# Kernel tuning notes

Measured on AMD Instinct MI355X. Metric: run time of the kernel, lower is better.

## Reference

```python
import math
import jax, jax.numpy as jnp
import numpy as np

EMBED = 512
HEADS = 2
HEAD_DIM = EMBED // HEADS


def setup_inputs() -> dict:
    key = jax.random.key(0)
    ks = jax.random.split(key, 10)
    s = 1.0 / math.sqrt(EMBED)
    return {
        "text_embeds": jax.random.normal(ks[0], (64, 32, EMBED), jnp.float32),
        "video_embeds": jax.random.normal(ks[1], (128, 64, EMBED), jnp.float32),
        "Wq": jax.random.normal(ks[2], (EMBED, EMBED), jnp.float32) * s,
        "bq": jnp.zeros((EMBED,), jnp.float32),
        "Wk": jax.random.normal(ks[3], (EMBED, EMBED), jnp.float32) * s,
        "bk": jnp.zeros((EMBED,), jnp.float32),
        "Wv": jax.random.normal(ks[4], (EMBED, EMBED), jnp.float32) * s,
        "bv": jnp.zeros((EMBED,), jnp.float32),
        "Wo": jax.random.normal(ks[5], (EMBED, EMBED), jnp.float32) * s,
        "bo": jnp.zeros((EMBED,), jnp.float32),
    }


def reference(text_embeds, video_embeds, Wq, bq, Wk, bk, Wv, bv, Wo, bo):
    num_texts, num_words, _ = text_embeds.shape
    num_vids, num_frames, _ = video_embeds.shape
    # projections (torch Linear: x @ W.T + b)
    q = (text_embeds @ Wq.T + bq).reshape(num_texts, num_words, HEADS, HEAD_DIM)
    k = (video_embeds @ Wk.T + bk).reshape(num_vids, num_frames, HEADS, HEAD_DIM)
    v = (video_embeds @ Wv.T + bv).reshape(num_vids, num_frames, HEADS, HEAD_DIM)
    # 5D cross attention logits: [vids, texts, heads, frames, words]
    logits = jnp.einsum('avhd,bthd->abhvt', k, q) / math.sqrt(HEAD_DIM)
    weights = jax.nn.softmax(logits, axis=3)  # softmax over frames
    attn = jnp.einsum('avhd,abhvt->abhtd', v, weights)  # [a,b,h,t,d]
    # faithful to torch: reshape (a,b,h,t,d) -> (a,b,t,h*d) in row-major order
    attn = attn.reshape(num_vids, num_texts, num_words, EMBED)
    attn = attn.mean(axis=0)  # [texts, words, embed]
    return attn @ Wo.T + bo
```

## Files before the change

kernel.cpp:

```cpp
#include <hip/hip_runtime.h>
#include <hip/hip_bf16.h>
#include <math.h>

#define EMBED  512
#define HEADS  2
#define HDIM   256
#define NTEXT  64
#define NWORD  32
#define NVID   128
#define NFRM   64

typedef __attribute__((ext_vector_type(8))) short      short8;
typedef __attribute__((ext_vector_type(8))) unsigned short ushort8;
typedef __attribute__((ext_vector_type(4))) float      float4v;
typedef __attribute__((ext_vector_type(4))) unsigned short ushort4v;

__device__ __forceinline__ unsigned short f2bf(float x) {
    __hip_bfloat16 h = __float2bfloat16(x);
    return *(unsigned short*)&h;
}
__device__ __forceinline__ float bf2f(unsigned short u) {
    __hip_bfloat16 h = *(__hip_bfloat16*)&u;
    return __bfloat162float(h);
}

__device__ __forceinline__ void gload_lds16(unsigned short* dst, const unsigned short* src) {
#if __has_builtin(__builtin_amdgcn_global_load_lds)
    __builtin_amdgcn_global_load_lds((const __attribute__((address_space(1))) void*)src,
                                     (__attribute__((address_space(3))) void*)dst,
                                     16, 0, 0);
#else
    *(ushort8*)dst = *(const ushort8*)src;
#endif
}

__global__ __launch_bounds__(256)
void cvt5(const float* __restrict__ s0, const float* __restrict__ s1,
          const float* __restrict__ s2, const float* __restrict__ s3,
          const float* __restrict__ s4, unsigned short* __restrict__ dst) {
    const int y = blockIdx.y;
    const float* s; size_t off; int n4;
    if (y == 0)      { s = s0; off = 0;       n4 = 262144;  }
    else if (y == 1) { s = s1; off = 1048576; n4 = 1048576; }
    else if (y == 2) { s = s2; off = 5242880; n4 = 65536;   }
    else if (y == 3) { s = s3; off = 5505024; n4 = 65536;   }
    else             { s = s4; off = 5767168; n4 = 65536;   }
    unsigned short* d = dst + off;
    for (int i = blockIdx.x * 256 + threadIdx.x; i < n4; i += 512 * 256) {
        float4v f = ((const float4v*)s)[i];
        ((ushort4v*)d)[i] = (ushort4v){f2bf(f.x), f2bf(f.y), f2bf(f.z), f2bf(f.w)};
    }
}

__global__ __launch_bounds__(256)
void proj_qkv(const unsigned short* __restrict__ text, const unsigned short* __restrict__ video,
              const unsigned short* __restrict__ Wqb, const float* __restrict__ bq,
              const unsigned short* __restrict__ Wkb, const float* __restrict__ bk,
              const unsigned short* __restrict__ Wvb, const float* __restrict__ bv,
              unsigned short* __restrict__ qout,
              unsigned short* __restrict__ Kgf, unsigned short* __restrict__ Vgf) {
    const int mb = blockIdx.x, nb = blockIdx.y;
    const int bj = nb * 128;
    const unsigned short *A, *W;
    const float* bias;
    int op, arow0, abase = 0;
    if (mb < 16)      { op = 0; A = text;  W = Wqb; bias = bq; arow0 = mb * 128; }
    else if (mb < 80) { op = 1; A = video; W = Wkb; bias = bk; abase = (mb - 16) * 2; arow0 = abase * 64; }
    else              { op = 2; A = video; W = Wvb; bias = bv; abase = (mb - 80) * 2; arow0 = abase * 64; }

    __shared__ __align__(16) unsigned char smem[65536];

    const int tid = threadIdx.x;
    const int w = tid >> 6, lane = tid & 63;
    const int lm = lane & 15, qd = lane >> 4;
    const int wr = w >> 1, wc = w & 1;

    float4v acc[4][4];
    #pragma unroll
    for (int rt = 0; rt < 4; ++rt)
        #pragma unroll
        for (int ct = 0; ct < 4; ++ct) acc[rt][ct] = (float4v){0.f, 0.f, 0.f, 0.f};

    auto STAGE = [&](int buf, int k0) {
        unsigned short* AbL = (unsigned short*)(smem + buf * 32768);
        unsigned short* WbL = (unsigned short*)(smem + buf * 32768 + 16384);
        #pragma unroll
        for (int it = 0; it < 4; ++it) {
            const int s = tid + it * 256;
            const int r = s >> 3, c8 = s & 7;
            const int sc = (c8 ^ (r & 7)) * 8;
            gload_lds16(&AbL[(size_t)s * 8], &A[(size_t)(arow0 + r) * 512 + k0 + sc]);
            gload_lds16(&WbL[(size_t)s * 8], &W[(size_t)(bj    + r) * 512 + k0 + sc]);
        }
    };

    STAGE(0, 0);
    __syncthreads();
    int cur = 0;
    for (int ks = 0; ks < 8; ++ks) {
        if (ks < 7) STAGE(cur ^ 1, (ks + 1) * 64);
        const unsigned short* AbL = (const unsigned short*)(smem + cur * 32768);
        const unsigned short* WbL = (const unsigned short*)(smem + cur * 32768 + 16384);
        #pragma unroll
        for (int kq = 0; kq < 2; ++kq) {
            const int scol = (kq * 32 + qd * 8) ^ ((lm & 7) * 8);
            short8 af[4], bf[4];
            #pragma unroll
            for (int rt = 0; rt < 4; ++rt)
                af[rt] = *(const short8*)&AbL[(wr * 64 + rt * 16 + lm) * 64 + scol];
            #pragma unroll
            for (int ct = 0; ct < 4; ++ct)
                bf[ct] = *(const short8*)&WbL[(wc * 64 + ct * 16 + lm) * 64 + scol];
            #pragma unroll
            for (int rt = 0; rt < 4; ++rt)
                #pragma unroll
                for (int ct = 0; ct < 4; ++ct)
                    acc[rt][ct] = __builtin_amdgcn_mfma_f32_16x16x32_bf16(af[rt], bf[ct], acc[rt][ct], 0, 0, 0);
        }
        __syncthreads();
        cur ^= 1;
    }

    if (op == 0) {
        #pragma unroll
        for (int rt = 0; rt < 4; ++rt)
            #pragma unroll
            for (int ct = 0; ct < 4; ++ct) {
                const int c = bj + wc * 64 + ct * 16 + lm;
                const float bb = bias[c];
                #pragma unroll
                for (int reg = 0; reg < 4; ++reg) {
                    const int r = arow0 + wr * 64 + rt * 16 + qd * 4 + reg;
                    qout[(size_t)r * 512 + c] = f2bf((acc[rt][ct][reg] + bb) * 0.0625f);
                }
            }
        return;
    }

    const int a   = abase + wr;
    const int bjs = bj + wc * 64;
    const int h      = bjs >> 8;
    const int bj_rel = bjs & 255;
    unsigned short (*Eb)[72] = (unsigned short (*)[72])(smem + w * 9216);
    const size_t base = ((size_t)(h * 128 + a)) * 16384;

    if (op == 1) {
        #pragma unroll
        for (int ct = 0; ct < 4; ++ct) {
            const int dl = ct * 16 + lm;
            const float bb = bias[bjs + dl];
            #pragma unroll
            for (int rt = 0; rt < 4; ++rt)
                #pragma unroll
                for (int reg = 0; reg < 4; ++reg)
                    Eb[rt * 16 + qd * 4 + reg][dl] = f2bf(acc[rt][ct][reg] + bb);
        }
        __syncthreads();
        #pragma unroll
        for (int it = 0; it < 8; ++it) {
            const int s = lane + it * 64;
            const int ntf = s >> 7, kqr = (s >> 6) & 1, l = s & 63;
            const int v = ntf * 16 + (l & 15);
            const int dl = kqr * 32 + (l >> 4) * 8;
            ushort8 val = *(const ushort8*)&Eb[v][dl];
            *(ushort8*)&Kgf[base + ((size_t)(ntf * 8 + (bj_rel >> 5) + kqr) * 64 + l) * 8] = val;
        }
    } else {
        #pragma unroll
        for (int ct = 0; ct < 4; ++ct) {
            const int dl = ct * 16 + lm;
            const float bb = bias[bjs + dl];
            #pragma unroll
            for (int rt = 0; rt < 4; ++rt)
                #pragma unroll
                for (int reg = 0; reg < 4; ++reg)
                    Eb[dl][rt * 16 + qd * 4 + reg] = f2bf(acc[rt][ct][reg] + bb);
        }
        __syncthreads();
        #pragma unroll
        for (int it = 0; it < 8; ++it) {
            const int s = lane + it * 64;
            const int ntr = s >> 7, kqv = (s >> 6) & 1, l = s & 63;
            const int dl = ntr * 16 + (l & 15);
            const int v0 = kqv * 32 + (l >> 4) * 8;
            ushort8 val = *(const ushort8*)&Eb[dl][v0];
            *(ushort8*)&Vgf[base + ((size_t)(((bj_rel >> 4) + ntr) * 2 + kqv) * 64 + l) * 8] = val;
        }
    }
}

__global__ __launch_bounds__(512, 2)
void attn9(const unsigned short* __restrict__ Kgf,
           const unsigned short* __restrict__ Vgf,
           const unsigned short* __restrict__ q,
           unsigned short* __restrict__ partg) {
    const int c  = blockIdx.x;
    const int h  = blockIdx.y;
    const int tg = blockIdx.z;
    const int tid = threadIdx.x;
    const int w = tid >> 6, lane = tid & 63;
    const int lm = lane & 15, qd = lane >> 4;
    const int wt = w >> 1;
    const int fh = w & 1;
    const int b = tg * 4 + wt;

    __shared__ __align__(16) unsigned short Kb[2][16384];
    __shared__ __align__(16) unsigned short Vb[2][16384];
    __shared__ __align__(16) unsigned short Pf[4][2][2][512];
    __shared__ __align__(16) float Ex[4][2][2][16][2];

    short8 qf[2][8];
    #pragma unroll
    for (int mt = 0; mt < 2; ++mt)
        #pragma unroll
        for (int kq = 0; kq < 8; ++kq)
            qf[mt][kq] = *(const short8*)
                &q[((size_t)(b * 32 + mt * 16 + lm)) * 512 + h * 256 + kq * 32 + qd * 8];

    float4v pacc[2][8];
    #pragma unroll
    for (int mt = 0; mt < 2; ++mt)
        #pragma unroll
        for (int nd = 0; nd < 8; ++nd) pacc[mt][nd] = (float4v){0.f, 0.f, 0.f, 0.f};

    const size_t vb0 = (size_t)(h * 128 + c * 16) * 16384;

    #pragma unroll
    for (int i = 0; i < 4; ++i) {
        const int s = tid + i * 512;
        gload_lds16(&Kb[0][(size_t)s * 8], &Kgf[vb0 + (size_t)s * 8]);
        gload_lds16(&Vb[0][(size_t)s * 8], &Vgf[vb0 + (size_t)s * 8]);
    }
    #pragma unroll
    for (int i = 0; i < 4; ++i) {
        const int s = tid + i * 512;
        gload_lds16(&Kb[1][(size_t)s * 8], &Kgf[vb0 + 16384 + (size_t)s * 8]);
        gload_lds16(&Vb[1][(size_t)s * 8], &Vgf[vb0 + 16384 + (size_t)s * 8]);
    }
    __syncthreads();

    for (int ai = 0; ai < 16; ++ai) {
        const int cur = ai & 1;

        float4v lacc[2][2];
        #pragma unroll
        for (int nt = 0; nt < 2; ++nt)
            #pragma unroll
            for (int mt = 0; mt < 2; ++mt) lacc[nt][mt] = (float4v){0.f, 0.f, 0.f, 0.f};
        #pragma unroll
        for (int kq = 0; kq < 8; ++kq) {
            #pragma unroll
            for (int nt = 0; nt < 2; ++nt) {
                const short8 kf = *(const short8*)
                    &Kb[cur][(((fh * 2 + nt) * 8 + kq) * 64 + lane) * 8];
                lacc[nt][0] = __builtin_amdgcn_mfma_f32_16x16x32_bf16(kf, qf[0][kq], lacc[nt][0], 0, 0, 0);
                lacc[nt][1] = __builtin_amdgcn_mfma_f32_16x16x32_bf16(kf, qf[1][kq], lacc[nt][1], 0, 0, 0);
            }
        }

        float m2[2], sv[2], e[2][2][4];
        #pragma unroll
        for (int mt = 0; mt < 2; ++mt) {
            float mm = lacc[0][mt][0];
            #pragma unroll
            for (int nt = 0; nt < 2; ++nt)
                #pragma unroll
                for (int r = 0; r < 4; ++r) mm = fmaxf(mm, lacc[nt][mt][r]);
            mm = fmaxf(mm, __shfl_xor(mm, 16));
            mm = fmaxf(mm, __shfl_xor(mm, 32));
            float ss = 0.f;
            #pragma unroll
            for (int nt = 0; nt < 2; ++nt)
                #pragma unroll
                for (int r = 0; r < 4; ++r) {
                    const float ev = __expf(lacc[nt][mt][r] - mm);
                    e[mt][nt][r] = ev;
                    ss += ev;
                }
            ss += __shfl_xor(ss, 16);
            ss += __shfl_xor(ss, 32);
            m2[mt] = mm; sv[mt] = ss;
            if (qd == 0) {
                Ex[wt][fh][mt][lm][0] = mm;
                Ex[wt][fh][mt][lm][1] = ss;
            }
        }
        __syncthreads();

        #pragma unroll
        for (int mt = 0; mt < 2; ++mt) {
            const float om = Ex[wt][fh ^ 1][mt][lm][0];
            const float os = Ex[wt][fh ^ 1][mt][lm][1];
            const float M   = fmaxf(m2[mt], om);
            const float den = sv[mt] * __expf(m2[mt] - M) + os * __expf(om - M);
            const float fac = __expf(m2[mt] - M) / den;
            #pragma unroll
            for (int nt = 0; nt < 2; ++nt) {
                ushort4v pv;
                pv.x = f2bf(e[mt][nt][0] * fac);
                pv.y = f2bf(e[mt][nt][1] * fac);
                pv.z = f2bf(e[mt][nt][2] * fac);
                pv.w = f2bf(e[mt][nt][3] * fac);
                *(ushort4v*)&Pf[wt][mt][fh][(lm + 16 * (nt * 2 + (qd >> 1))) * 8 + (qd & 1) * 4] = pv;
            }
        }
        __syncthreads();

        #pragma unroll
        for (int kqv = 0; kqv < 2; ++kqv) {
            const short8 pf0 = *(const short8*)&Pf[wt][0][kqv][lane * 8];
            const short8 pf1 = *(const short8*)&Pf[wt][1][kqv][lane * 8];
            #pragma unroll
            for (int nd = 0; nd < 8; ++nd) {
                const short8 vf = *(const short8*)
                    &Vb[cur][(((fh * 8 + nd) * 2 + kqv) * 64 + lane) * 8];
                pacc[0][nd] = __builtin_amdgcn_mfma_f32_16x16x32_bf16(pf0, vf, pacc[0][nd], 0, 0, 0);
                pacc[1][nd] = __builtin_amdgcn_mfma_f32_16x16x32_bf16(pf1, vf, pacc[1][nd], 0, 0, 0);
            }
        }
        __syncthreads();

        if (ai < 14) {
            const size_t kb = vb0 + (size_t)(ai + 2) * 16384;
            #pragma unroll
            for (int i = 0; i < 4; ++i) {
                const int s = tid + i * 512;
                gload_lds16(&Kb[cur][(size_t)s * 8], &Kgf[kb + (size_t)s * 8]);
                gload_lds16(&Vb[cur][(size_t)s * 8], &Vgf[kb + (size_t)s * 8]);
            }
        }
    }

    unsigned short* part = partg + (size_t)c * 1048576;
    #pragma unroll
    for (int mt = 0; mt < 2; ++mt)
        #pragma unroll
        for (int nd = 0; nd < 8; ++nd)
            #pragma unroll
            for (int r = 0; r < 4; ++r) {
                const int t = mt * 16 + qd * 4 + r;
                const int d = fh * 128 + nd * 16 + lm;
                const int row = b * 32 + h * 16 + (t >> 1);
                const int col = (t & 1) * 256 + d;
                part[(size_t)row * 512 + col] = f2bf(pacc[mt][nd][r]);
            }
}

__global__ __launch_bounds__(256)
void reduce8(unsigned short* __restrict__ partg) {
    const size_t i = ((size_t)blockIdx.x * 256 + threadIdx.x) * 8;
    float s[8];
    #pragma unroll
    for (int j = 0; j < 8; ++j) s[j] = 0.f;
    #pragma unroll
    for (int p = 0; p < 8; ++p) {
        ushort8 u = *(const ushort8*)&partg[(size_t)p * 1048576 + i];
        #pragma unroll
        for (int j = 0; j < 8; ++j) s[j] += bf2f(u[j]);
    }
    ushort8 o;
    #pragma unroll
    for (int j = 0; j < 8; ++j) o[j] = f2bf(s[j] * 0.0078125f);
    *(ushort8*)&partg[i] = o;
}

__global__ __launch_bounds__(256)
void proj_o(const unsigned short* __restrict__ Abf, const float* __restrict__ W,
            const float* __restrict__ bias, float* __restrict__ C) {
    __shared__ __align__(16) unsigned short Ab[64][72];
    __shared__ __align__(16) unsigned short Wb[64][72];
    const int tid = threadIdx.x;
    const int bi = blockIdx.x * 64, bj = blockIdx.y * 64;
    const int w = tid >> 6, lane = tid & 63;
    const int lm = lane & 15, qd = lane >> 4;

    float4v acc[4];
    #pragma unroll
    for (int nt = 0; nt < 4; ++nt) acc[nt] = (float4v){0.f, 0.f, 0.f, 0.f};

    for (int k0 = 0; k0 < 512; k0 += 64) {
        #pragma unroll
        for (int it = 0; it < 2; ++it) {
            const int s = tid + it * 256;
            const int r = s >> 3, c8 = (s & 7) * 8;
            *(ushort8*)&Ab[r][c8] = *(const ushort8*)&Abf[(size_t)(bi + r) * 512 + k0 + c8];
        }
        #pragma unroll
        for (int it = 0; it < 4; ++it) {
            const int s = tid + it * 256;
            const int r = s >> 4, c4 = (s & 15) * 4;
            float4v fw = *(const float4v*)&W[(size_t)(bj + r) * 512 + k0 + c4];
            *(ushort4v*)&Wb[r][c4] = (ushort4v){f2bf(fw.x), f2bf(fw.y), f2bf(fw.z), f2bf(fw.w)};
        }
        __syncthreads();
        #pragma unroll
        for (int kq = 0; kq < 2; ++kq) {
            const short8 af = *(const short8*)&Ab[w * 16 + lm][kq * 32 + qd * 8];
            #pragma unroll
            for (int nt = 0; nt < 4; ++nt) {
                const short8 bf = *(const short8*)&Wb[nt * 16 + lm][kq * 32 + qd * 8];
                acc[nt] = __builtin_amdgcn_mfma_f32_16x16x32_bf16(af, bf, acc[nt], 0, 0, 0);
            }
        }
        __syncthreads();
    }
    #pragma unroll
    for (int nt = 0; nt < 4; ++nt) {
        const int cc = bj + nt * 16 + lm;
        const float bb = bias[cc];
        #pragma unroll
        for (int reg = 0; reg < 4; ++reg) {
            const int r = bi + w * 16 + qd * 4 + reg;
            C[(size_t)r * 512 + cc] = acc[nt][reg] + bb;
        }
    }
}

extern "C" void kernel_launch(void* const* d_in, const int* in_sizes, int n_in,
                              void* d_out, int out_size, void* d_ws, size_t ws_size,
                              hipStream_t stream) {
    const float* text  = (const float*)d_in[0];
    const float* video = (const float*)d_in[1];
    const float* Wq = (const float*)d_in[2];
    const float* bq = (const float*)d_in[3];
    const float* Wk = (const float*)d_in[4];
    const float* bk = (const float*)d_in[5];
    const float* Wv = (const float*)d_in[6];
    const float* bv = (const float*)d_in[7];
    const float* Wo = (const float*)d_in[8];
    const float* bo = (const float*)d_in[9];

    unsigned short* Kgf   = (unsigned short*)d_ws;
    unsigned short* Vgf   = (unsigned short*)((char*)d_ws + (8u << 20));
    unsigned short* partg = (unsigned short*)((char*)d_ws + (16u << 20));
    unsigned short* textbf  = partg;
    unsigned short* videobf = partg + 1048576;
    unsigned short* wqbf    = partg + 5242880;
    unsigned short* wkbf    = partg + 5505024;
    unsigned short* wvbf    = partg + 5767168;
    unsigned short* qbf   = (unsigned short*)d_out;
    float*          out   = (float*)d_out;

    cvt5<<<dim3(512, 5), 256, 0, stream>>>(text, video, Wq, Wk, Wv, partg);
    proj_qkv<<<dim3(144, 4), 256, 0, stream>>>(textbf, videobf, wqbf, bq, wkbf, bk,
                                               wvbf, bv, qbf, Kgf, Vgf);
    attn9<<<dim3(8, 2, 16), 512, 0, stream>>>(Kgf, Vgf, qbf, partg);
    reduce8<<<dim3(512), 256, 0, stream>>>(partg);
    proj_o<<<dim3(32, 8), 256, 0, stream>>>(partg, Wo, bo, out);
}
```

Measured before the change: 167.1 us.

## Fuse all five stages into one cooperative persistent kernel with grid syncs

Replaces the five separate launches (convert, QKV projection, attention, reduce, output projection) with one cooperative kernel of 256 blocks of 512 threads that steps through the stages separated by grid.sync(). Each block runs two 256-thread contexts for the projection jobs and reuses the attention and output-projection code with remapped block indices. The aim is to cut launch overhead and the idle gaps between kernels. In exchange it adds grid-wide barrier costs, uses about 146 KB of LDS per block, and fixes the per-stage parallelism at 256 blocks, which may leave stages load-imbalanced.

```diff
diff --git a/kernel.cpp b/kernel.cpp
--- a/kernel.cpp
+++ b/kernel.cpp
@@ -1,6 +1,9 @@
 #include <hip/hip_runtime.h>
+#include <hip/hip_cooperative_groups.h>
 #include <hip/hip_bf16.h>
 #include <math.h>
+
+namespace cg = cooperative_groups;
 
 #define EMBED  512
 #define HEADS  2
@@ -34,384 +37,403 @@
 #endif
 }
 
-__global__ __launch_bounds__(256)
-void cvt5(const float* __restrict__ s0, const float* __restrict__ s1,
-          const float* __restrict__ s2, const float* __restrict__ s3,
-          const float* __restrict__ s4, unsigned short* __restrict__ dst) {
-    const int y = blockIdx.y;
-    const float* s; size_t off; int n4;
-    if (y == 0)      { s = s0; off = 0;       n4 = 262144;  }
-    else if (y == 1) { s = s1; off = 1048576; n4 = 1048576; }
-    else if (y == 2) { s = s2; off = 5242880; n4 = 65536;   }
-    else if (y == 3) { s = s3; off = 5505024; n4 = 65536;   }
-    else             { s = s4; off = 5767168; n4 = 65536;   }
-    unsigned short* d = dst + off;
-    for (int i = blockIdx.x * 256 + threadIdx.x; i < n4; i += 512 * 256) {
-        float4v f = ((const float4v*)s)[i];
-        ((ushort4v*)d)[i] = (ushort4v){f2bf(f.x), f2bf(f.y), f2bf(f.z), f2bf(f.w)};
+__global__ __launch_bounds__(512, 2)
+void mega(const float* __restrict__ text, const float* __restrict__ video,
+          const float* __restrict__ Wq, const float* __restrict__ bq,
+          const float* __restrict__ Wk, const float* __restrict__ bk,
+          const float* __restrict__ Wv, const float* __restrict__ bv,
+          const float* __restrict__ Wo, const float* __restrict__ bo,
+          unsigned short* qbf,
+          unsigned short* __restrict__ Kgf, unsigned short* __restrict__ Vgf,
+          unsigned short* partg,
+          float* out)
+{
+    cg::grid_group grid = cg::this_grid();
+    __shared__ __align__(16) unsigned char smem[149504];
+    const int bid = blockIdx.x;
+    const int tid = threadIdx.x;
+
+    unsigned short* textbf  = partg;
+    unsigned short* videobf = partg + 1048576;
+    unsigned short* wqbf    = partg + 5242880;
+    unsigned short* wkbf    = partg + 5505024;
+    unsigned short* wvbf    = partg + 5767168;
+
+    {
+        const int gidx = bid * 512 + tid;
+        #pragma unroll
+        for (int rgn = 0; rgn < 5; ++rgn) {
+            const float* s = (rgn == 0) ? text : (rgn == 1) ? video
+                            : (rgn == 2) ? Wq : (rgn == 3) ? Wk : Wv;
+            const int off = (rgn == 0) ? 0 : (rgn == 1) ? 1048576
+                            : (rgn == 2) ? 5242880 : (rgn == 3) ? 5505024 : 5767168;
+            const int n4 = (rgn == 0) ? 262144 : (rgn == 1) ? 1048576 : 65536;
+            unsigned short* d = partg + off;
+            for (int i = gidx; i < n4; i += 131072) {
+                float4v f = ((const float4v*)s)[i];
+                ((ushort4v*)d)[i] = (ushort4v){f2bf(f.x), f2bf(f.y), f2bf(f.z), f2bf(f.w)};
+            }
+        }
     }
-}
-
-__global__ __launch_bounds__(256)
-void proj_qkv(const unsigned short* __restrict__ text, const unsigned short* __restrict__ video,
-              const unsigned short* __restrict__ Wqb, const float* __restrict__ bq,
-              const unsigned short* __restrict__ Wkb, const float* __restrict__ bk,
-              const unsigned short* __restrict__ Wvb, const float* __restrict__ bv,
-              unsigned short* __restrict__ qout,
-              unsigned short* __restrict__ Kgf, unsigned short* __restrict__ Vgf) {
-    const int mb = blockIdx.x, nb = blockIdx.y;
-    const int bj = nb * 128;
-    const unsigned short *A, *W;
-    const float* bias;
-    int op, arow0, abase = 0;
-    if (mb < 16)      { op = 0; A = text;  W = Wqb; bias = bq; arow0 = mb * 128; }
-    else if (mb < 80) { op = 1; A = video; W = Wkb; bias = bk; abase = (mb - 16) * 2; arow0 = abase * 64; }
-    else              { op = 2; A = video; W = Wvb; bias = bv; abase = (mb - 80) * 2; arow0 = abase * 64; }
-
-    __shared__ __align__(16) unsigned char smem[65536];
-
-    const int tid = threadIdx.x;
-    const int w = tid >> 6, lane = tid & 63;
-    const int lm = lane & 15, qd = lane >> 4;
-    const int wr = w >> 1, wc = w & 1;
-
-    float4v acc[4][4];
-    #pragma unroll
-    for (int rt = 0; rt < 4; ++rt)
-        #pragma unroll
-        for (int ct = 0; ct < 4; ++ct) acc[rt][ct] = (float4v){0.f, 0.f, 0.f, 0.f};
-
-    auto STAGE = [&](int buf, int k0) {
-        unsigned short* AbL = (unsigned short*)(smem + buf * 32768);
-        unsigned short* WbL = (unsigned short*)(smem + buf * 32768 + 16384);
-        #pragma unroll
-        for (int it = 0; it < 4; ++it) {
-            const int s = tid + it * 256;
-            const int r = s >> 3, c8 = s & 7;
-            const int sc = (c8 ^ (r & 7)) * 8;
-            gload_lds16(&AbL[(size_t)s * 8], &A[(size_t)(arow0 + r) * 512 + k0 + sc]);
-            gload_lds16(&WbL[(size_t)s * 8], &W[(size_t)(bj    + r) * 512 + k0 + sc]);
-        }
-    };
-
-    STAGE(0, 0);
-    __syncthreads();
-    int cur = 0;
-    for (int ks = 0; ks < 8; ++ks) {
-        if (ks < 7) STAGE(cur ^ 1, (ks + 1) * 64);
-        const unsigned short* AbL = (const unsigned short*)(smem + cur * 32768);
-        const unsigned short* WbL = (const unsigned short*)(smem + cur * 32768 + 16384);
-        #pragma unroll
-        for (int kq = 0; kq < 2; ++kq) {
-            const int scol = (kq * 32 + qd * 8) ^ ((lm & 7) * 8);
-            short8 af[4], bf[4];
+    grid.sync();
+
+    {
+        const int ctxL = tid >> 8;
+        const int vt = tid & 255;
+        unsigned char* cs = smem + ctxL * 65536;
+        const int ctxId = bid * 2 + ctxL;
+        const int w = vt >> 6, lane = vt & 63;
+        const int lm = lane & 15, qd = lane >> 4;
+        const int wr = w >> 1, wc = w & 1;
+
+        for (int jr = 0; jr < 2; ++jr) {
+            if (jr == 1 && bid >= 32) break;
+            const int job = (jr == 0) ? ctxId : 512 + ctxId;
+            const int mb = job % 144, nb = job / 144;
+            const int bj = nb * 128;
+            const unsigned short *A, *W;
+            const float* bias;
+            int op, arow0, abase = 0;
+            if (mb < 16)      { op = 0; A = textbf;  W = wqbf; bias = bq; arow0 = mb * 128; }
+            else if (mb < 80) { op = 1; A = videobf; W = wkbf; bias = bk; abase = (mb - 16) * 2; arow0 = abase * 64; }
+            else              { op = 2; A = videobf; W = wvbf; bias = bv; abase = (mb - 80) * 2; arow0 = abase * 64; }
+
+            float4v acc[4][4];
             #pragma unroll
             for (int rt = 0; rt < 4; ++rt)
-                af[rt] = *(const short8*)&AbL[(wr * 64 + rt * 16 + lm) * 64 + scol];
-            #pragma unroll
-            for (int ct = 0; ct < 4; ++ct)
-                bf[ct] = *(const short8*)&WbL[(wc * 64 + ct * 16 + lm) * 64 + scol];
-            #pragma unroll
-            for (int rt = 0; rt < 4; ++rt)
-                #pragma unroll
-                for (int ct = 0; ct < 4; ++ct)
-                    acc[rt][ct] = __builtin_amdgcn_mfma_f32_16x16x32_bf16(af[rt], bf[ct], acc[rt][ct], 0, 0, 0);
+                #pragma unroll
+                for (int ct = 0; ct < 4; ++ct) acc[rt][ct] = (float4v){0.f, 0.f, 0.f, 0.f};
+
+            auto STAGE = [&](int buf, int k0) {
+                unsigned short* AbL = (unsigned short*)(cs + buf * 32768);
+                unsigned short* WbL = (unsigned short*)(cs + buf * 32768 + 16384);
+                #pragma unroll
+                for (int it = 0; it < 4; ++it) {
+                    const int s = vt + it * 256;
+                    const int r = s >> 3, c8 = s & 7;
+                    const int sc = (c8 ^ (r & 7)) * 8;
+                    gload_lds16(&AbL[(size_t)s * 8], &A[(size_t)(arow0 + r) * 512 + k0 + sc]);
+                    gload_lds16(&WbL[(size_t)s * 8], &W[(size_t)(bj    + r) * 512 + k0 + sc]);
+                }
+            };
+
+            STAGE(0, 0);
+            __syncthreads();
+            int cur = 0;
+            for (int ks = 0; ks < 8; ++ks) {
+                if (ks < 7) STAGE(cur ^ 1, (ks + 1) * 64);
+                const unsigned short* AbL = (const unsigned short*)(cs + cur * 32768);
+                const unsigned short* WbL = (const unsigned short*)(cs + cur * 32768 + 16384);
+                #pragma unroll
+                for (int kq = 0; kq < 2; ++kq) {
+                    const int scol = (kq * 32 + qd * 8) ^ ((lm & 7) * 8);
+                    short8 af[4], bf[4];
+                    #pragma unroll
+                    for (int rt = 0; rt < 4; ++rt)
+                        af[rt] = *(const short8*)&AbL[(wr * 64 + rt * 16 + lm) * 64 + scol];
+                    #pragma unroll
+                    for (int ct = 0; ct < 4; ++ct)
+                        bf[ct] = *(const short8*)&WbL[(wc * 64 + ct * 16 + lm) * 64 + scol];
+                    #pragma unroll
+                    for (int rt = 0; rt < 4; ++rt)
+                        #pragma unroll
+                        for (int ct = 0; ct < 4; ++ct)
+                            acc[rt][ct] = __builtin_amdgcn_mfma_f32_16x16x32_bf16(af[rt], bf[ct], acc[rt][ct], 0, 0, 0);
+                }
+                __syncthreads();
+                cur ^= 1;
+            }
+
+            if (op == 0) {
+                __syncthreads();
+                #pragma unroll
+                for (int rt = 0; rt < 4; ++rt)
+                    #pragma unroll
+                    for (int ct = 0; ct < 4; ++ct) {
+                        const int cc = bj + wc * 64 + ct * 16 + lm;
+                        const float bb = bias[cc];
+                        #pragma unroll
+                        for (int reg = 0; reg < 4; ++reg) {
+                            const int r = arow0 + wr * 64 + rt * 16 + qd * 4 + reg;
+                            qbf[(size_t)r * 512 + cc] = f2bf((acc[rt][ct][reg] + bb) * 0.0625f);
+                        }
+                    }
+            } else {
+                const int a   = abase + wr;
+                const int bjs = bj + wc * 64;
+                const int h      = bjs >> 8;
+                const int bj_rel = bjs & 255;
+                unsigned short (*Eb)[72] = (unsigned short (*)[72])(cs + w * 9216);
+                const size_t base = ((size_t)(h * 128 + a)) * 16384;
+                if (op == 1) {
+                    #pragma unroll
+                    for (int ct = 0; ct < 4; ++ct) {
+                        const int dl = ct * 16 + lm;
+                        const float bb = bias[bjs + dl];
+                        #pragma unroll
+                        for (int rt = 0; rt < 4; ++rt)
+                            #pragma unroll
+                            for (int reg = 0; reg < 4; ++reg)
+                                Eb[rt * 16 + qd * 4 + reg][dl] = f2bf(acc[rt][ct][reg] + bb);
+                    }
+                    __syncthreads();
+                    #pragma unroll
+                    for (int it = 0; it < 8; ++it) {
+                        const int s = lane + it * 64;
+                        const int ntf = s >> 7, kqr = (s >> 6) & 1, l = s & 63;
+                        const int v = ntf * 16 + (l & 15);
+                        const int dl = kqr * 32 + (l >> 4) * 8;
+                        ushort8 val = *(const ushort8*)&Eb[v][dl];
+                        *(ushort8*)&Kgf[base + ((size_t)(ntf * 8 + (bj_rel >> 5) + kqr) * 64 + l) * 8] = val;
+                    }
+                } else {
+                    #pragma unroll
+                    for (int ct = 0; ct < 4; ++ct) {
+                        const int dl = ct * 16 + lm;
+                        const float bb = bias[bjs + dl];
+                        #pragma unroll
+                        for (int rt = 0; rt < 4; ++rt)
+                            #pragma unroll
+                            for (int reg = 0; reg < 4; ++reg)
+                                Eb[dl][rt * 16 + qd * 4 + reg] = f2bf(acc[rt][ct][reg] + bb);
+                    }
+                    __syncthreads();
+                    #pragma unroll
+                    for (int it = 0; it < 8; ++it) {
+                        const int s = lane + it * 64;
+                        const int ntr = s >> 7, kqv = (s >> 6) & 1, l = s & 63;
+                        const int dl = ntr * 16 + (l & 15);
+                        const int v0 = kqv * 32 + (l >> 4) * 8;
+                        ushort8 val = *(const ushort8*)&Eb[dl][v0];
+                        *(ushort8*)&Vgf[base + ((size_t)(((bj_rel >> 4) + ntr) * 2 + kqv) * 64 + l) * 8] = val;
+                    }
+                }
+            }
+            __syncthreads();
+        }
+    }
+    grid.sync();
+
+    {
+        const int c = bid & 7, h = (bid >> 3) & 1, tg = bid >> 4;
+        const int w = tid >> 6, lane = tid & 63;
+        const int lm = lane & 15, qd = lane >> 4;
+        const int wt = w >> 1, fh = w & 1;
+        const int b = tg * 4 + wt;
+
+        unsigned short* KbA = (unsigned short*)smem;
+        unsigned short* VbA = (unsigned short*)(smem + 65536);
+        unsigned short* PfA = (unsigned short*)(smem + 131072);
+        float*          ExA = (float*)(smem + 147456);
+
+        short8 qf[2][8];
+        #pragma unroll
+        for (int mt = 0; mt < 2; ++mt)
+            #pragma unroll
+            for (int kq = 0; kq < 8; ++kq)
+                qf[mt][kq] = *(const short8*)
+                    &qbf[((size_t)(b * 32 + mt * 16 + lm)) * 512 + h * 256 + kq * 32 + qd * 8];
+
+        float4v pacc[2][8];
+        #pragma unroll
+        for (int mt = 0; mt < 2; ++mt)
+            #pragma unroll
+            for (int nd = 0; nd < 8; ++nd) pacc[mt][nd] = (float4v){0.f, 0.f, 0.f, 0.f};
+
+        const size_t vb0 = (size_t)(h * 128 + c * 16) * 16384;
+
+        #pragma unroll
+        for (int i = 0; i < 4; ++i) {
+            const int s = tid + i * 512;
+            gload_lds16(&KbA[(size_t)s * 8], &Kgf[vb0 + (size_t)s * 8]);
+            gload_lds16(&VbA[(size_t)s * 8], &Vgf[vb0 + (size_t)s * 8]);
+        }
+        #pragma unroll
+        for (int i = 0; i < 4; ++i) {
+            const int s = tid + i * 512;
+            gload_lds16(&KbA[16384 + (size_t)s * 8], &Kgf[vb0 + 16384 + (size_t)s * 8]);
+            gload_lds16(&VbA[16384 + (size_t)s * 8], &Vgf[vb0 + 16384 + (size_t)s * 8]);
         }
         __syncthreads();
-        cur ^= 1;
+
+        for (int ai = 0; ai < 16; ++ai) {
+            const int cur = ai & 1;
+            const unsigned short* Kc = KbA + cur * 16384;
+            const unsigned short* Vc = VbA + cur * 16384;
+
+            float4v lacc[2][2];
+            #pragma unroll
+            for (int nt = 0; nt < 2; ++nt)
+                #pragma unroll
+                for (int mt = 0; mt < 2; ++mt) lacc[nt][mt] = (float4v){0.f, 0.f, 0.f, 0.f};
+            #pragma unroll
+            for (int kq = 0; kq < 8; ++kq) {
+                #pragma unroll
+                for (int nt = 0; nt < 2; ++nt) {
+                    const short8 kf = *(const short8*)
+                        &Kc[(((fh * 2 + nt) * 8 + kq) * 64 + lane) * 8];
+                    lacc[nt][0] = __builtin_amdgcn_mfma_f32_16x16x32_bf16(kf, qf[0][kq], lacc[nt][0], 0, 0, 0);
+                    lacc[nt][1] = __builtin_amdgcn_mfma_f32_16x16x32_bf16(kf, qf[1][kq], lacc[nt][1], 0, 0, 0);
+                }
+            }
+
+            float m2[2], sv[2], e[2][2][4];
+            #pragma unroll
+            for (int mt = 0; mt < 2; ++mt) {
+                float mm = lacc[0][mt][0];
+                #pragma unroll
+                for (int nt = 0; nt < 2; ++nt)
+                    #pragma unroll
+                    for (int r = 0; r < 4; ++r) mm = fmaxf(mm, lacc[nt][mt][r]);
+                mm = fmaxf(mm, __shfl_xor(mm, 16));
+                mm = fmaxf(mm, __shfl_xor(mm, 32));
+                float ss = 0.f;
+                #pragma unroll
+                for (int nt = 0; nt < 2; ++nt)
+                    #pragma unroll
+                    for (int r = 0; r < 4; ++r) {
+                        const float ev = __expf(lacc[nt][mt][r] - mm);
+                        e[mt][nt][r] = ev;
+                        ss += ev;
+                    }
+                ss += __shfl_xor(ss, 16);
+                ss += __shfl_xor(ss, 32);
+                m2[mt] = mm; sv[mt] = ss;
+                if (qd == 0) {
+                    ExA[(((wt * 2 + fh) * 2 + mt) * 16 + lm) * 2 + 0] = mm;
+                    ExA[(((wt * 2 + fh) * 2 + mt) * 16 + lm) * 2 + 1] = ss;
+                }
+            }
+            __syncthreads();
+
+            #pragma unroll
+            for (int mt = 0; mt < 2; ++mt) {
+                const float om = ExA[(((wt * 2 + (fh ^ 1)) * 2 + mt) * 16 + lm) * 2 + 0];
+                const float os = ExA[(((wt * 2 + (fh ^ 1)) * 2 + mt) * 16 + lm) * 2 + 1];
+                const float M   = fmaxf(m2[mt], om);
+                const float den = sv[mt] * __expf(m2[mt] - M) + os * __expf(om - M);
+                const float fac = __expf(m2[mt] - M) / den;
+                #pragma unroll
+                for (int nt = 0; nt < 2; ++nt) {
+                    ushort4v pv;
+                    pv.x = f2bf(e[mt][nt][0] * fac);
+                    pv.y = f2bf(e[mt][nt][1] * fac);
+                    pv.z = f2bf(e[mt][nt][2] * fac);
+                    pv.w = f2bf(e[mt][nt][3] * fac);
+                    *(ushort4v*)&PfA[((wt * 2 + mt) * 2 + fh) * 512
+                                     + (lm + 16 * (nt * 2 + (qd >> 1))) * 8 + (qd & 1) * 4] = pv;
+                }
+            }
+            __syncthreads();
+
+            #pragma unroll
+            for (int kqv = 0; kqv < 2; ++kqv) {
+                const short8 pf0 = *(const short8*)&PfA[((wt * 2 + 0) * 2 + kqv) * 512 + lane * 8];
+                const short8 pf1 = *(const short8*)&PfA[((wt * 2 + 1) * 2 + kqv) * 512 + lane * 8];
+                #pragma unroll
+                for (int nd = 0; nd < 8; ++nd) {
+                    const short8 vf = *(const short8*)
+                        &Vc[(((fh * 8 + nd) * 2 + kqv) * 64 + lane) * 8];
+                    pacc[0][nd] = __builtin_amdgcn_mfma_f32_16x16x32_bf16(pf0, vf, pacc[0][nd], 0, 0, 0);
+                    pacc[1][nd] = __builtin_amdgcn_mfma_f32_16x16x32_bf16(pf1, vf, pacc[1][nd], 0, 0, 0);
+                }
+            }
+            __syncthreads();
+
+            if (ai < 14) {
+                const size_t kb = vb0 + (size_t)(ai + 2) * 16384;
+                #pragma unroll
+                for (int i = 0; i < 4; ++i) {
+                    const int s = tid + i * 512;
+                    gload_lds16(&KbA[cur * 16384 + (size_t)s * 8], &Kgf[kb + (size_t)s * 8]);
+                    gload_lds16(&VbA[cur * 16384 + (size_t)s * 8], &Vgf[kb + (size_t)s * 8]);
+                }
+            }
+        }
+
+        unsigned short* part = partg + (size_t)c * 1048576;
+        #pragma unroll
+        for (int mt = 0; mt < 2; ++mt)
+            #pragma unroll
+            for (int nd = 0; nd < 8; ++nd)
+                #pragma unroll
+                for (int r = 0; r < 4; ++r) {
+                    const int t = mt * 16 + qd * 4 + r;
+                    const int d = fh * 128 + nd * 16 + lm;
+                    const int row = b * 32 + h * 16 + (t >> 1);
+                    const int col = (t & 1) * 256 + d;
+                    part[(size_t)row * 512 + col] = f2bf(pacc[mt][nd][r]);
+                }
     }
-
-    if (op == 0) {
-        #pragma unroll
-        for (int rt = 0; rt < 4; ++rt)
-            #pragma unroll
-            for (int ct = 0; ct < 4; ++ct) {
-                const int c = bj + wc * 64 + ct * 16 + lm;
-                const float bb = bias[c];
-                #pragma unroll
-                for (int reg = 0; reg < 4; ++reg) {
-                    const int r = arow0 + wr * 64 + rt * 16 + qd * 4 + reg;
-                    qout[(size_t)r * 512 + c] = f2bf((acc[rt][ct][reg] + bb) * 0.0625f);
-                }
-            }
-        return;
+    grid.sync();
+
+    {
+        const size_t i = ((size_t)bid * 512 + tid) * 8;
+        float s[8];
+        #pragma unroll
+        for (int j = 0; j < 8; ++j) s[j] = 0.f;
+        #pragma unroll
+        for (int p = 0; p < 8; ++p) {
+            ushort8 u = *(const ushort8*)&partg[(size_t)p * 1048576 + i];
+            #pragma unroll
+            for (int j = 0; j < 8; ++j) s[j] += bf2f(u[j]);
+        }
+        ushort8 o;
+        #pragma unroll
+        for (int j = 0; j < 8; ++j) o[j] = f2bf(s[j] * 0.0078125f);
+        *(ushort8*)&partg[i] = o;
     }
-
-    const int a   = abase + wr;
-    const int bjs = bj + wc * 64;
-    const int h      = bjs >> 8;
-    const int bj_rel = bjs & 255;
-    unsigned short (*Eb)[72] = (unsigned short (*)[72])(smem + w * 9216);
-    const size_t base = ((size_t)(h * 128 + a)) * 16384;
-
-    if (op == 1) {
-        #pragma unroll
-        for (int ct = 0; ct < 4; ++ct) {
-            const int dl = ct * 16 + lm;
-            const float bb = bias[bjs + dl];
-            #pragma unroll
-            for (int rt = 0; rt < 4; ++rt)
-                #pragma unroll
-                for (int reg = 0; reg < 4; ++reg)
-                    Eb[rt * 16 + qd * 4 + reg][dl] = f2bf(acc[rt][ct][reg] + bb);
-        }
-        __syncthreads();
-        #pragma unroll
-        for (int it = 0; it < 8; ++it) {
-            const int s = lane + it * 64;
-            const int ntf = s >> 7, kqr = (s >> 6) & 1, l = s & 63;
-            const int v = ntf * 16 + (l & 15);
-            const int dl = kqr * 32 + (l >> 4) * 8;
-            ushort8 val = *(const ushort8*)&Eb[v][dl];
-            *(ushort8*)&Kgf[base + ((size_t)(ntf * 8 + (bj_rel >> 5) + kqr) * 64 + l) * 8] = val;
-        }
-    } else {
-        #pragma unroll
-        for (int ct = 0; ct < 4; ++ct) {
-            const int dl = ct * 16 + lm;
-            const float bb = bias[bjs + dl];
-            #pragma unroll
-            for (int rt = 0; rt < 4; ++rt)
-                #pragma unroll
-                for (int reg = 0; reg < 4; ++reg)
-                    Eb[dl][rt * 16 + qd * 4 + reg] = f2bf(acc[rt][ct][reg] + bb);
-        }
-        __syncthreads();
-        #pragma unroll
-        for (int it = 0; it < 8; ++it) {
-            const int s = lane + it * 64;
-            const int ntr = s >> 7, kqv = (s >> 6) & 1, l = s & 63;
-            const int dl = ntr * 16 + (l & 15);
-            const int v0 = kqv * 32 + (l >> 4) * 8;
-            ushort8 val = *(const ushort8*)&Eb[dl][v0];
-            *(ushort8*)&Vgf[base + ((size_t)(((bj_rel >> 4) + ntr) * 2 + kqv) * 64 + l) * 8] = val;
-        }
-    }
-}
-
-__global__ __launch_bounds__(512, 2)
-void attn9(const unsigned short* __restrict__ Kgf,
-           const unsigned short* __restrict__ Vgf,
-           const unsigned short* __restrict__ q,
-           unsigned short* __restrict__ partg) {
-    const int c  = blockIdx.x;
-    const int h  = blockIdx.y;
-    const int tg = blockIdx.z;
-    const int tid = threadIdx.x;
-    const int w = tid >> 6, lane = tid & 63;
-    const int lm = lane & 15, qd = lane >> 4;
-    const int wt = w >> 1;
-    const int fh = w & 1;
-    const int b = tg * 4 + wt;
-
-    __shared__ __align__(16) unsigned short Kb[2][16384];
-    __shared__ __align__(16) unsigned short Vb[2][16384];
-    __shared__ __align__(16) unsigned short Pf[4][2][2][512];
-    __shared__ __align__(16) float Ex[4][2][2][16][2];
-
-    short8 qf[2][8];
-    #pragma unroll
-    for (int mt = 0; mt < 2; ++mt)
-        #pragma unroll
-        for (int kq = 0; kq < 8; ++kq)
-            qf[mt][kq] = *(const short8*)
-                &q[((size_t)(b * 32 + mt * 16 + lm)) * 512 + h * 256 + kq * 32 + qd * 8];
-
-    float4v pacc[2][8];
-    #pragma unroll
-    for (int mt = 0; mt < 2; ++mt)
-        #pragma unroll
-        for (int nd = 0; nd < 8; ++nd) pacc[mt][nd] = (float4v){0.f, 0.f, 0.f, 0.f};
-
-    const size_t vb0 = (size_t)(h * 128 + c * 16) * 16384;
-
-    #pragma unroll
-    for (int i = 0; i < 4; ++i) {
-        const int s = tid + i * 512;
-        gload_lds16(&Kb[0][(size_t)s * 8], &Kgf[vb0 + (size_t)s * 8]);
-        gload_lds16(&Vb[0][(size_t)s * 8], &Vgf[vb0 + (size_t)s * 8]);
-    }
-    #pragma unroll
-    for (int i = 0; i < 4; ++i) {
-        const int s = tid + i * 512;
-        gload_lds16(&Kb[1][(size_t)s * 8], &Kgf[vb0 + 16384 + (size_t)s * 8]);
-        gload_lds16(&Vb[1][(size_t)s * 8], &Vgf[vb0 + 16384 + (size_t)s * 8]);
-    }
-    __syncthreads();
-
-    for (int ai = 0; ai < 16; ++ai) {
-        const int cur = ai & 1;
-
-        float4v lacc[2][2];
-        #pragma unroll
-        for (int nt = 0; nt < 2; ++nt)
-            #pragma unroll
-            for (int mt = 0; mt < 2; ++mt) lacc[nt][mt] = (float4v){0.f, 0.f, 0.f, 0.f};
-        #pragma unroll
-        for (int kq = 0; kq < 8; ++kq) {
-            #pragma unroll
-            for (int nt = 0; nt < 2; ++nt) {
-                const short8 kf = *(const short8*)
-                    &Kb[cur][(((fh * 2 + nt) * 8 + kq) * 64 + lane) * 8];
-                lacc[nt][0] = __builtin_amdgcn_mfma_f32_16x16x32_bf16(kf, qf[0][kq], lacc[nt][0], 0, 0, 0);
-                lacc[nt][1] = __builtin_amdgcn_mfma_f32_16x16x32_bf16(kf, qf[1][kq], lacc[nt][1], 0, 0, 0);
-            }
-        }
-
-        float m2[2], sv[2], e[2][2][4];
-        #pragma unroll
-        for (int mt = 0; mt < 2; ++mt) {
-            float mm = lacc[0][mt][0];
-            #pragma unroll
-            for (int nt = 0; nt < 2; ++nt)
-                #pragma unroll
-                for (int r = 0; r < 4; ++r) mm = fmaxf(mm, lacc[nt][mt][r]);
-            mm = fmaxf(mm, __shfl_xor(mm, 16));
-            mm = fmaxf(mm, __shfl_xor(mm, 32));
-            float ss = 0.f;
-            #pragma unroll
-            for (int nt = 0; nt < 2; ++nt)
-                #pragma unroll
-                for (int r = 0; r < 4; ++r) {
-                    const float ev = __expf(lacc[nt][mt][r] - mm);
-                    e[mt][nt][r] = ev;
-                    ss += ev;
-                }
-            ss += __shfl_xor(ss, 16);
-            ss += __shfl_xor(ss, 32);
-            m2[mt] = mm; sv[mt] = ss;
-            if (qd == 0) {
-                Ex[wt][fh][mt][lm][0] = mm;
-                Ex[wt][fh][mt][lm][1] = ss;
-            }
-        }
-        __syncthreads();
-
-        #pragma unroll
-        for (int mt = 0; mt < 2; ++mt) {
-            const float om = Ex[wt][fh ^ 1][mt][lm][0];
-            const float os = Ex[wt][fh ^ 1][mt][lm][1];
-            const float M   = fmaxf(m2[mt], om);
-            const float den = sv[mt] * __expf(m2[mt] - M) + os * __expf(om - M);
-            const float fac = __expf(m2[mt] - M) / den;
-            #pragma unroll
-            for (int nt = 0; nt < 2; ++nt) {
-                ushort4v pv;
-                pv.x = f2bf(e[mt][nt][0] * fac);
-                pv.y = f2bf(e[mt][nt][1] * fac);
-                pv.z = f2bf(e[mt][nt][2] * fac);
-                pv.w = f2bf(e[mt][nt][3] * fac);
-                *(ushort4v*)&Pf[wt][mt][fh][(lm + 16 * (nt * 2 + (qd >> 1))) * 8 + (qd & 1) * 4] = pv;
-            }
-        }
-        __syncthreads();
-
-        #pragma unroll
-        for (int kqv = 0; kqv < 2; ++kqv) {
-            const short8 pf0 = *(const short8*)&Pf[wt][0][kqv][lane * 8];
-            const short8 pf1 = *(const short8*)&Pf[wt][1][kqv][lane * 8];
-            #pragma unroll
-            for (int nd = 0; nd < 8; ++nd) {
-                const short8 vf = *(const short8*)
-                    &Vb[cur][(((fh * 8 + nd) * 2 + kqv) * 64 + lane) * 8];
-                pacc[0][nd] = __builtin_amdgcn_mfma_f32_16x16x32_bf16(pf0, vf, pacc[0][nd], 0, 0, 0);
-                pacc[1][nd] = __builtin_amdgcn_mfma_f32_16x16x32_bf16(pf1, vf, pacc[1][nd], 0, 0, 0);
-            }
-        }
-        __syncthreads();
-
-        if (ai < 14) {
-            const size_t kb = vb0 + (size_t)(ai + 2) * 16384;
-            #pragma unroll
-            for (int i = 0; i < 4; ++i) {
-                const int s = tid + i * 512;
-                gload_lds16(&Kb[cur][(size_t)s * 8], &Kgf[kb + (size_t)s * 8]);
-                gload_lds16(&Vb[cur][(size_t)s * 8], &Vgf[kb + (size_t)s * 8]);
-            }
-        }
-    }
-
-    unsigned short* part = partg + (size_t)c * 1048576;
-    #pragma unroll
-    for (int mt = 0; mt < 2; ++mt)
-        #pragma unroll
-        for (int nd = 0; nd < 8; ++nd)
-            #pragma unroll
-            for (int r = 0; r < 4; ++r) {
-                const int t = mt * 16 + qd * 4 + r;
-                const int d = fh * 128 + nd * 16 + lm;
-                const int row = b * 32 + h * 16 + (t >> 1);
-                const int col = (t & 1) * 256 + d;
-                part[(size_t)row * 512 + col] = f2bf(pacc[mt][nd][r]);
-            }
-}
-
-__global__ __launch_bounds__(256)
-void reduce8(unsigned short* __restrict__ partg) {
-    const size_t i = ((size_t)blockIdx.x * 256 + threadIdx.x) * 8;
-    float s[8];
-    #pragma unroll
-    for (int j = 0; j < 8; ++j) s[j] = 0.f;
-    #pragma unroll
-    for (int p = 0; p < 8; ++p) {
-        ushort8 u = *(const ushort8*)&partg[(size_t)p * 1048576 + i];
-        #pragma unroll
-        for (int j = 0; j < 8; ++j) s[j] += bf2f(u[j]);
-    }
-    ushort8 o;
-    #pragma unroll
-    for (int j = 0; j < 8; ++j) o[j] = f2bf(s[j] * 0.0078125f);
-    *(ushort8*)&partg[i] = o;
-}
-
-__global__ __launch_bounds__(256)
-void proj_o(const unsigned short* __restrict__ Abf, const float* __restrict__ W,
-            const float* __restrict__ bias, float* __restrict__ C) {
-    __shared__ __align__(16) unsigned short Ab[64][72];
-    __shared__ __align__(16) unsigned short Wb[64][72];
-    const int tid = threadIdx.x;
-    const int bi = blockIdx.x * 64, bj = blockIdx.y * 64;
-    const int w = tid >> 6, lane = tid & 63;
-    const int lm = lane & 15, qd = lane >> 4;
-
-    float4v acc[4];
-    #pragma unroll
-    for (int nt = 0; nt < 4; ++nt) acc[nt] = (float4v){0.f, 0.f, 0.f, 0.f};
-
-    for (int k0 = 0; k0 < 512; k0 += 64) {
-        #pragma unroll
-        for (int it = 0; it < 2; ++it) {
-            const int s = tid + it * 256;
-            const int r = s >> 3, c8 = (s & 7) * 8;
-            *(ushort8*)&Ab[r][c8] = *(const ushort8*)&Abf[(size_t)(bi + r) * 512 + k0 + c8];
-        }
-        #pragma unroll
-        for (int it = 0; it < 4; ++it) {
-            const int s = tid + it * 256;
-            const int r = s >> 4, c4 = (s & 15) * 4;
-            float4v fw = *(const float4v*)&W[(size_t)(bj + r) * 512 + k0 + c4];
-            *(ushort4v*)&Wb[r][c4] = (ushort4v){f2bf(fw.x), f2bf(fw.y), f2bf(fw.z), f2bf(fw.w)};
-        }
-        __syncthreads();
-        #pragma unroll
-        for (int kq = 0; kq < 2; ++kq) {
-            const short8 af = *(const short8*)&Ab[w * 16 + lm][kq * 32 + qd * 8];
-            #pragma unroll
-            for (int nt = 0; nt < 4; ++nt) {
-                const short8 bf = *(const short8*)&Wb[nt * 16 + lm][kq * 32 + qd * 8];
-                acc[nt] = __builtin_amdgcn_mfma_f32_16x16x32_bf16(af, bf, acc[nt], 0, 0, 0);
-            }
-        }
-        __syncthreads();
-    }
-    #pragma unroll
-    for (int nt = 0; nt < 4; ++nt) {
-        const int cc = bj + nt * 16 + lm;
-        const float bb = bias[cc];
-        #pragma unroll
-        for (int reg = 0; reg < 4; ++reg) {
-            const int r = bi + w * 16 + qd * 4 + reg;
-            C[(size_t)r * 512 + cc] = acc[nt][reg] + bb;
+    grid.sync();
+
+    if (bid < 128) {
+        const int ctxL = tid >> 8;
+        const int vt = tid & 255;
+        const int w = vt >> 6, lane = vt & 63;
+        const int lm = lane & 15, qd = lane >> 4;
+        const int bi = (bid >> 2) * 64;
+        const int bj = (bid & 3) * 128 + ctxL * 64;
+        unsigned short (*Ab)[72] = (unsigned short (*)[72])(smem + ctxL * 18432);
+        unsigned short (*Wb)[72] = (unsigned short (*)[72])(smem + ctxL * 18432 + 9216);
+
+        float4v acc[4];
+        #pragma unroll
+        for (int nt = 0; nt < 4; ++nt) acc[nt] = (float4v){0.f, 0.f, 0.f, 0.f};
+
+        for (int k0 = 0; k0 < 512; k0 += 64) {
+            #pragma unroll
+            for (int it = 0; it < 2; ++it) {
+                const int s = vt + it * 256;
+                const int r = s >> 3, c8 = (s & 7) * 8;
+                *(ushort8*)&Ab[r][c8] = *(const ushort8*)&partg[(size_t)(bi + r) * 512 + k0 + c8];
+            }
+            #pragma unroll
+            for (int it = 0; it < 4; ++it) {
+                const int s = vt + it * 256;
+                const int r = s >> 4, c4 = (s & 15) * 4;
+                float4v fw = *(const float4v*)&Wo[(size_t)(bj + r) * 512 + k0 + c4];
+                *(ushort4v*)&Wb[r][c4] = (ushort4v){f2bf(fw.x), f2bf(fw.y), f2bf(fw.z), f2bf(fw.w)};
+            }
+            __syncthreads();
+            #pragma unroll
+            for (int kq = 0; kq < 2; ++kq) {
+                const short8 af = *(const short8*)&Ab[w * 16 + lm][kq * 32 + qd * 8];
+                #pragma unroll
+                for (int nt = 0; nt < 4; ++nt) {
+                    const short8 bfr = *(const short8*)&Wb[nt * 16 + lm][kq * 32 + qd * 8];
+                    acc[nt] = __builtin_amdgcn_mfma_f32_16x16x32_bf16(af, bfr, acc[nt], 0, 0, 0);
+                }
+            }
+            __syncthreads();
+        }
+        #pragma unroll
+        for (int nt = 0; nt < 4; ++nt) {
+            const int cc = bj + nt * 16 + lm;
+            const float bb = bo[cc];
+            #pragma unroll
+            for (int reg = 0; reg < 4; ++reg) {
+                const int r = bi + w * 16 + qd * 4 + reg;
+                out[(size_t)r * 512 + cc] = acc[nt][reg] + bb;
+            }
         }
     }
 }
@@ -433,18 +455,13 @@
     unsigned short* Kgf   = (unsigned short*)d_ws;
     unsigned short* Vgf   = (unsigned short*)((char*)d_ws + (8u << 20));
     unsigned short* partg = (unsigned short*)((char*)d_ws + (16u << 20));
-    unsigned short* textbf  = partg;
-    unsigned short* videobf = partg + 1048576;
-    unsigned short* wqbf    = partg + 5242880;
-    unsigned short* wkbf    = partg + 5505024;
-    unsigned short* wvbf    = partg + 5767168;
     unsigned short* qbf   = (unsigned short*)d_out;
     float*          out   = (float*)d_out;
 
-    cvt5<<<dim3(512, 5), 256, 0, stream>>>(text, video, Wq, Wk, Wv, partg);
-    proj_qkv<<<dim3(144, 4), 256, 0, stream>>>(textbf, videobf, wqbf, bq, wkbf, bk,
-                                               wvbf, bv, qbf, Kgf, Vgf);
-    attn9<<<dim3(8, 2, 16), 512, 0, stream>>>(Kgf, Vgf, qbf, partg);
-    reduce8<<<dim3(512), 256, 0, stream>>>(partg);
-    proj_o<<<dim3(32, 8), 256, 0, stream>>>(partg, Wo, bo, out);
+    void* args[] = {(void*)&text, (void*)&video, (void*)&Wq, (void*)&bq,
+                    (void*)&Wk, (void*)&bk, (void*)&Wv, (void*)&bv,
+                    (void*)&Wo, (void*)&bo, (void*)&qbf, (void*)&Kgf,
+                    (void*)&Vgf, (void*)&partg, (void*)&out};
+    hipLaunchCooperativeKernel((const void*)mega, dim3(256), dim3(512),
+                               args, 0, stream);
 }
```

After: 327.6 us. 96.1% more time.
